# Kernel optimization log

Hardware: AMD Instinct MI355X
Metric: run time of the kernel (lower is better)

## Reference

```python
import jax, jax.numpy as jnp
import numpy as np

N, E, F_IN, C1, H1, C2, NUM_CLASSES, NUM_GRAPHS = 50000, 800000, 128, 64, 4, 128, 5, 32
NEG_SLOPE = 0.2


def gat_conv(x, W, att_src, att_dst, bias, src, dst, heads, out_ch):
    # x: [N, in], W: [in, heads*out_ch], att_*: [heads, out_ch], bias: [heads*out_ch]
    n = x.shape[0]
    h = (x @ W).reshape(n, heads, out_ch)                      # [N,H,C]
    a_src = jnp.sum(h * att_src, axis=-1)                      # [N,H]
    a_dst = jnp.sum(h * att_dst, axis=-1)                      # [N,H]
    alpha = a_src[src] + a_dst[dst]                            # [E,H]
    alpha = jax.nn.leaky_relu(alpha, NEG_SLOPE)
    # scatter-softmax over incoming edges of each dst node (every node has a self-loop)
    amax = jax.ops.segment_max(alpha, dst, num_segments=n)
    ealpha = jnp.exp(alpha - amax[dst])
    denom = jax.ops.segment_sum(ealpha, dst, num_segments=n)
    alpha = ealpha / (denom[dst] + 1e-16)                      # [E,H]
    msg = h[src] * alpha[..., None]                            # [E,H,C]
    out = jax.ops.segment_sum(msg, dst, num_segments=n)        # [N,H,C]
    return out.reshape(n, heads * out_ch) + bias


def setup_inputs() -> dict:
    key = jax.random.key(0)
    ks = jax.random.split(key, 12)
    x = jax.random.normal(ks[0], (N, F_IN), dtype=jnp.float32)
    edge_index = jax.random.randint(ks[1], (2, E), 0, N, dtype=jnp.int64)
    batch = jnp.sort(jax.random.randint(ks[2], (N,), 0, NUM_GRAPHS, dtype=jnp.int64))
    s1 = 1.0 / np.sqrt(F_IN)
    s2 = 1.0 / np.sqrt(H1 * C1)
    s3 = 1.0 / np.sqrt(C2)
    return {
        "x": x,
        "edge_index": edge_index,
        "batch": batch,
        "W1": jax.random.normal(ks[3], (F_IN, H1 * C1), dtype=jnp.float32) * s1,
        "att_src1": jax.random.normal(ks[4], (H1, C1), dtype=jnp.float32) * s1,
        "att_dst1": jax.random.normal(ks[5], (H1, C1), dtype=jnp.float32) * s1,
        "b1": jnp.zeros((H1 * C1,), dtype=jnp.float32),
        "W2": jax.random.normal(ks[6], (H1 * C1, C2), dtype=jnp.float32) * s2,
        "att_src2": jax.random.normal(ks[7], (1, C2), dtype=jnp.float32) * s2,
        "att_dst2": jax.random.normal(ks[8], (1, C2), dtype=jnp.float32) * s2,
        "b2": jnp.zeros((C2,), dtype=jnp.float32),
        "lin_w": jax.random.normal(ks[9], (C2, NUM_CLASSES), dtype=jnp.float32) * s3,
        "lin_b": jnp.zeros((NUM_CLASSES,), dtype=jnp.float32),
    }


def reference(x, edge_index, batch, W1, att_src1, att_dst1, b1, W2, att_src2, att_dst2, b2, lin_w, lin_b):
    n = x.shape[0]
    # PyG GATConv adds self-loops by default
    loops = jnp.arange(n, dtype=edge_index.dtype)
    src = jnp.concatenate([edge_index[0], loops])
    dst = jnp.concatenate([edge_index[1], loops])
    h = jax.nn.elu(gat_conv(x, W1, att_src1, att_dst1, b1, src, dst, H1, C1))
    h = jax.nn.elu(gat_conv(h, W2, att_src2, att_dst2, b2, src, dst, 1, C2))
    # global_mean_pool over graphs
    sums = jax.ops.segment_sum(h, batch, num_segments=NUM_GRAPHS)          # [G,C2]
    counts = jax.ops.segment_sum(jnp.ones((n,), h.dtype), batch, num_segments=NUM_GRAPHS)
    pooled = sums / jnp.maximum(counts, 1.0)[:, None]
    # dropout is identity in eval mode
    return pooled @ lin_w + lin_b
```

## Files before the change

### kernel.cpp

```cpp
#include <hip/hip_runtime.h>
#include <math.h>

#define NEG_SLOPE 0.2f

__device__ inline float lrelu(float x) { return x > 0.f ? x : NEG_SLOPE * x; }

typedef __attribute__((ext_vector_type(8))) _Float16 f16x8;
typedef __attribute__((ext_vector_type(4))) float f32x4;
typedef __attribute__((ext_vector_type(2))) float f32x2;
typedef __attribute__((ext_vector_type(4))) _Float16 h16x4;
typedef __attribute__((ext_vector_type(2))) _Float16 h16x2;

__global__ void convW_k(const float* __restrict__ W1, const float* __restrict__ W2,
                        _Float16* __restrict__ BT1, _Float16* __restrict__ BT2)
{
    int i = blockIdx.x * blockDim.x + threadIdx.x;
    if (i < 32768) {
        int n = i >> 7, k = i & 127;
        BT1[(size_t)n * 128 + k] = (_Float16)W1[(size_t)k * 256 + n];
    } else {
        int idx = i - 32768;
        int n = idx >> 8, k = idx & 255;
        BT2[(size_t)n * 256 + k] = (_Float16)W2[(size_t)k * 128 + n];
    }
}

template<int N, int K, int H, bool AF16>
__launch_bounds__(256)
__global__ void gemm_fused(const void* __restrict__ A, const _Float16* __restrict__ BT,
                           unsigned char* __restrict__ HB, const float* __restrict__ att_s,
                           const float* __restrict__ att_d, float* __restrict__ aS,
                           float* __restrict__ aD, int M)
{
    constexpr int ITERS = K / 32;
    constexpr int WN = N / 4;
    constexpr int NT = WN / 16;
    constexpr int NCH = (N * 4) / 256;
    __shared__ unsigned short As[64 * 40] __attribute__((aligned(16)));
    __shared__ unsigned short Bs[N * 40] __attribute__((aligned(16)));
    const int t = threadIdx.x;
    const int wave = t >> 6, lane = t & 63;
    const int quad = lane >> 4, l15 = lane & 15;
    const int rowBase = blockIdx.x * 64;

    f32x4 acc[4][NT];
#pragma unroll
    for (int mi = 0; mi < 4; ++mi)
#pragma unroll
        for (int ni = 0; ni < NT; ++ni)
            acc[mi][ni] = (f32x4){0.f, 0.f, 0.f, 0.f};

    const int ar = t >> 2;
    const int ak = (t & 3) << 3;
    const int bc = (t * NCH) >> 2;
    const int bks = (t * NCH) & 3;

    for (int it = 0; it < ITERS; ++it) {
        {
            int gr = rowBase + ar;
            f16x8 hv;
#pragma unroll
            for (int j = 0; j < 8; ++j) hv[j] = (_Float16)0.f;
            if (gr < M) {
                if constexpr (AF16) {
                    hv = *(const f16x8*)((const _Float16*)A + (size_t)gr * K + it * 32 + ak);
                } else {
                    const float* ap = (const float*)A + (size_t)gr * K + it * 32 + ak;
                    float4 v0 = *(const float4*)ap;
                    float4 v1 = *(const float4*)(ap + 4);
                    hv[0] = (_Float16)v0.x; hv[1] = (_Float16)v0.y;
                    hv[2] = (_Float16)v0.z; hv[3] = (_Float16)v0.w;
                    hv[4] = (_Float16)v1.x; hv[5] = (_Float16)v1.y;
                    hv[6] = (_Float16)v1.z; hv[7] = (_Float16)v1.w;
                }
            }
            *(f16x8*)&As[ar * 40 + ak] = hv;
        }
        {
            const _Float16* bp = BT + (size_t)bc * K + it * 32 + bks * 8;
            unsigned short* dp = &Bs[bc * 40 + bks * 8];
#pragma unroll
            for (int j = 0; j < NCH; ++j)
                *(f16x8*)(dp + j * 8) = *(const f16x8*)(bp + j * 8);
        }
        __syncthreads();
        f16x8 af[4], bfr[NT];
#pragma unroll
        for (int mi = 0; mi < 4; ++mi)
            af[mi] = *(const f16x8*)&As[(mi * 16 + l15) * 40 + quad * 8];
#pragma unroll
        for (int ni = 0; ni < NT; ++ni)
            bfr[ni] = *(const f16x8*)&Bs[(wave * WN + ni * 16 + l15) * 40 + quad * 8];
#pragma unroll
        for (int mi = 0; mi < 4; ++mi)
#pragma unroll
            for (int ni = 0; ni < NT; ++ni)
                acc[mi][ni] = __builtin_amdgcn_mfma_f32_16x16x32_f16(
                    af[mi], bfr[ni], acc[mi][ni], 0, 0, 0);
        __syncthreads();
    }
    float asv[NT], adv[NT];
#pragma unroll
    for (int ni = 0; ni < NT; ++ni) {
        int col = wave * WN + ni * 16 + l15;
        asv[ni] = att_s[col];
        adv[ni] = att_d[col];
    }
#pragma unroll
    for (int mi = 0; mi < 4; ++mi) {
#pragma unroll
        for (int r = 0; r < 4; ++r) {
            int row = rowBase + mi * 16 + quad * 4 + r;
            bool ok = row < M;
            float ss = 0.f, sd = 0.f;
#pragma unroll
            for (int ni = 0; ni < NT; ++ni) {
                float v = acc[mi][ni][r];
                ss += v * asv[ni];
                sd += v * adv[ni];
            }
#pragma unroll
            for (int ni = 0; ni < NT; ni += 2) {
                int pk = __builtin_amdgcn_cvt_pk_fp8_f32(acc[mi][ni][r],
                                                         acc[mi][ni + 1][r], 0, false);
                if (ok) {
                    HB[(size_t)row * N + wave * WN + ni * 16 + l15] =
                        (unsigned char)(pk & 0xff);
                    HB[(size_t)row * N + wave * WN + (ni + 1) * 16 + l15] =
                        (unsigned char)((pk >> 8) & 0xff);
                }
            }
#pragma unroll
            for (int off = 8; off > 0; off >>= 1) {
                ss += __shfl_xor(ss, off);
                sd += __shfl_xor(sd, off);
            }
            if (ok && l15 == 0) {
                if (H == 4) {
                    aS[row * 4 + wave] = ss;
                    aD[row * 4 + wave] = sd;
                } else {
                    atomicAdd(&aS[row], ss);
                    atomicAdd(&aD[row], sd);
                }
            }
        }
    }
}

#define BIN_EPT 32
__launch_bounds__(256)
__global__ void bcount_k(const int* __restrict__ dst, int* __restrict__ bcnt,
                         int ET, int E, int NBUCK)
{
    __shared__ int hist[1024];
    for (int i = threadIdx.x; i < NBUCK; i += 256) hist[i] = 0;
    __syncthreads();
    int e0 = blockIdx.x * (256 * BIN_EPT) + threadIdx.x;
#pragma unroll
    for (int j = 0; j < BIN_EPT; ++j) {
        int e = e0 + j * 256;
        if (e < ET) {
            int d = (e < E) ? dst[e] : (e - E);
            atomicAdd(&hist[d >> 6], 1);
        }
    }
    __syncthreads();
    for (int i = threadIdx.x; i < NBUCK; i += 256) {
        int c = hist[i];
        if (c > 0) atomicAdd(&bcnt[i], c);
    }
}

__global__ void bscan_k(const int* __restrict__ bcnt, int* __restrict__ bbase,
                        int* __restrict__ ccursor, int nb)
{
    __shared__ int sh[1024];
    int t = threadIdx.x;
    int v = (t < nb) ? bcnt[t] : 0;
    sh[t] = v;
    __syncthreads();
#pragma unroll
    for (int o = 1; o < 1024; o <<= 1) {
        int u = (t >= o) ? sh[t - o] : 0;
        __syncthreads();
        sh[t] += u;
        __syncthreads();
    }
    if (t < nb) {
        int excl = sh[t] - v;
        bbase[t] = excl;
        ccursor[t] = excl;
    }
    if (t == nb - 1) bbase[nb] = sh[t];
}

__launch_bounds__(256)
__global__ void binpass_k(const int* __restrict__ src, const int* __restrict__ dst,
                          int* __restrict__ ccursor, unsigned int* __restrict__ tmp,
                          int ET, int E, int NBUCK)
{
    __shared__ int hist[1024];
    for (int i = threadIdx.x; i < NBUCK; i += 256) hist[i] = 0;
    __syncthreads();
    int e0 = blockIdx.x * (256 * BIN_EPT) + threadIdx.x;
    unsigned int ev[BIN_EPT];
    int meta[BIN_EPT];
#pragma unroll
    for (int j = 0; j < BIN_EPT; ++j) {
        int e = e0 + j * 256;
        meta[j] = -1;
        if (e < ET) {
            int s, d;
            if (e < E) { s = src[e]; d = dst[e]; } else { s = e - E; d = s; }
            ev[j] = (unsigned int)s | ((unsigned int)d << 16);
            int b = d >> 6;
            int r = atomicAdd(&hist[b], 1);
            meta[j] = (r << 10) | b;
        }
    }
    __syncthreads();
    for (int i = threadIdx.x; i < NBUCK; i += 256) {
        int c = hist[i];
        hist[i] = (c > 0) ? atomicAdd(&ccursor[i], c) : 0;
    }
    __syncthreads();
#pragma unroll
    for (int j = 0; j < BIN_EPT; ++j) {
        if (meta[j] >= 0) {
            int b = meta[j] & 1023;
            int r = meta[j] >> 10;
            tmp[hist[b] + r] = ev[j];
        }
    }
}

__global__ void fine_k(const int* __restrict__ bbase, const unsigned int* __restrict__ tmp,
                       int* __restrict__ rowptr, unsigned short* __restrict__ esrc,
                       int Nn, int ET, int NBUCK)
{
    __shared__ int lcnt[64], lpre[64], lcur[64];
    int t = threadIdx.x;
    int b = blockIdx.x;
    int n0 = b << 6;
    int base = bbase[b];
    int end = bbase[b + 1];
    if (t < 64) lcnt[t] = 0;
    __syncthreads();
    for (int i = base + t; i < end; i += 256)
        atomicAdd(&lcnt[(tmp[i] >> 16) & 63], 1);
    __syncthreads();
    if (t < 64) lpre[t] = lcnt[t];
    __syncthreads();
#pragma unroll
    for (int o = 1; o < 64; o <<= 1) {
        int u = (t < 64 && t >= o) ? lpre[t - o] : 0;
        __syncthreads();
        if (t < 64) lpre[t] += u;
        __syncthreads();
    }
    if (t < 64) {
        int n = n0 + t;
        int excl = lpre[t] - lcnt[t];
        if (n < Nn) {
            rowptr[n] = base + excl;
            lcur[t] = base + excl;
        }
    }
    if (b == NBUCK - 1 && t == 0) rowptr[Nn] = ET;
    __syncthreads();
    for (int i = base + t; i < end; i += 256) {
        unsigned int v = tmp[i];
        int pos = atomicAdd(&lcur[(v >> 16) & 63], 1);
        esrc[pos] = (unsigned short)(v & 0xffffu);
    }
}

__global__ void gather1_k(const int* __restrict__ rp, const unsigned short* __restrict__ esrc,
                          const unsigned char* __restrict__ hb, const float* __restrict__ aS,
                          const float* __restrict__ aD, const float* __restrict__ bias,
                          _Float16* __restrict__ out, int Nn)
{
    int d = blockIdx.x * 4 + (threadIdx.x >> 6);
    int lane = threadIdx.x & 63;
    if (d >= Nn) return;
    int c4 = lane << 2;
    int head = lane >> 4;
    int p0 = __builtin_amdgcn_readfirstlane(rp[d]);
    int p1 = __builtin_amdgcn_readfirstlane(rp[d + 1]);
    float adh = aD[d * 4 + head];
    const float* aSh = aS + head;
    float m = -1e30f, den = 0.f;
    float ax = 0.f, ay = 0.f, az = 0.f, aw = 0.f;
    int p = p0;
    for (; p + 8 <= p1; p += 8) {
        int s[8];
#pragma unroll
        for (int j = 0; j < 8; ++j) s[j] = __builtin_amdgcn_readfirstlane(esrc[p + j]);
        unsigned int v[8];
#pragma unroll
        for (int j = 0; j < 8; ++j)
            v[j] = *(const unsigned int*)&hb[(size_t)s[j] * 256 + c4];
        float l[8];
#pragma unroll
        for (int j = 0; j < 8; ++j) l[j] = lrelu(aSh[s[j] * 4] + adh);
        float lm = l[0];
#pragma unroll
        for (int j = 1; j < 8; ++j) lm = fmaxf(lm, l[j]);
        if (lm > m) {
            float r = __expf(m - lm);
            ax *= r; ay *= r; az *= r; aw *= r; den *= r;
            m = lm;
        }
#pragma unroll
        for (int j = 0; j < 8; ++j) {
            float w = __expf(l[j] - m);
            den += w;
            f32x2 lo = __builtin_amdgcn_cvt_pk_f32_fp8((int)v[j], false);
            f32x2 hi = __builtin_amdgcn_cvt_pk_f32_fp8((int)v[j], true);
            ax += lo[0] * w;
            ay += lo[1] * w;
            az += hi[0] * w;
            aw += hi[1] * w;
        }
    }
    int rem = p1 - p;
    if (rem > 0) {
        int s[8];
        unsigned int v[8];
        float l[8];
#pragma unroll
        for (int j = 0; j < 8; ++j)
            if (j < rem) s[j] = __builtin_amdgcn_readfirstlane(esrc[p + j]);
#pragma unroll
        for (int j = 0; j < 8; ++j)
            if (j < rem) v[j] = *(const unsigned int*)&hb[(size_t)s[j] * 256 + c4];
#pragma unroll
        for (int j = 0; j < 8; ++j) l[j] = -1e30f;
#pragma unroll
        for (int j = 0; j < 8; ++j)
            if (j < rem) l[j] = lrelu(aSh[s[j] * 4] + adh);
        float lm = l[0];
#pragma unroll
        for (int j = 1; j < 8; ++j) lm = fmaxf(lm, l[j]);
        if (lm > m) {
            float r = __expf(m - lm);
            ax *= r; ay *= r; az *= r; aw *= r; den *= r;
            m = lm;
        }
#pragma unroll
        for (int j = 0; j < 8; ++j) {
            if (j < rem) {
                float w = __expf(l[j] - m);
                den += w;
                f32x2 lo = __builtin_amdgcn_cvt_pk_f32_fp8((int)v[j], false);
                f32x2 hi = __builtin_amdgcn_cvt_pk_f32_fp8((int)v[j], true);
                ax += lo[0] * w;
                ay += lo[1] * w;
                az += hi[0] * w;
                aw += hi[1] * w;
            }
        }
    }
    float inv = 1.f / (den + 1e-16f);
    float4 b4 = *(const float4*)&bias[c4];
    float rx, ry, rz, rw;
    rx = ax * inv + b4.x; rx = rx > 0.f ? rx : expm1f(rx);
    ry = ay * inv + b4.y; ry = ry > 0.f ? ry : expm1f(ry);
    rz = az * inv + b4.z; rz = rz > 0.f ? rz : expm1f(rz);
    rw = aw * inv + b4.w; rw = rw > 0.f ? rw : expm1f(rw);
    h16x4 r16;
    r16[0] = (_Float16)rx; r16[1] = (_Float16)ry;
    r16[2] = (_Float16)rz; r16[3] = (_Float16)rw;
    *(h16x4*)&out[(size_t)d * 256 + c4] = r16;
}

__global__ void gather2_k(const int* __restrict__ rp, const unsigned short* __restrict__ esrc,
                          const unsigned char* __restrict__ hb, const float* __restrict__ aS,
                          const float* __restrict__ aD, _Float16* __restrict__ out, int Nn)
{
    int d = blockIdx.x * 4 + (threadIdx.x >> 6);
    int lane = threadIdx.x & 63;
    if (d >= Nn) return;
    int c2 = lane << 1;
    int p0 = __builtin_amdgcn_readfirstlane(rp[d]);
    int p1 = __builtin_amdgcn_readfirstlane(rp[d + 1]);
    float adh = aD[d];
    float m = -1e30f, den = 0.f;
    float ax = 0.f, ay = 0.f;
    int p = p0;
    for (; p + 8 <= p1; p += 8) {
        int s[8];
#pragma unroll
        for (int j = 0; j < 8; ++j) s[j] = __builtin_amdgcn_readfirstlane(esrc[p + j]);
        unsigned short v[8];
#pragma unroll
        for (int j = 0; j < 8; ++j)
            v[j] = *(const unsigned short*)&hb[(size_t)s[j] * 128 + c2];
        float l[8];
#pragma unroll
        for (int j = 0; j < 8; ++j) l[j] = lrelu(aS[s[j]] + adh);
        float lm = l[0];
#pragma unroll
        for (int j = 1; j < 8; ++j) lm = fmaxf(lm, l[j]);
        if (lm > m) {
            float r = __expf(m - lm);
            ax *= r; ay *= r; den *= r;
            m = lm;
        }
#pragma unroll
        for (int j = 0; j < 8; ++j) {
            float w = __expf(l[j] - m);
            den += w;
            f32x2 lo = __builtin_amdgcn_cvt_pk_f32_fp8((int)v[j], false);
            ax += lo[0] * w;
            ay += lo[1] * w;
        }
    }
    int rem = p1 - p;
    if (rem > 0) {
        int s[8];
        unsigned short v[8];
        float l[8];
#pragma unroll
        for (int j = 0; j < 8; ++j)
            if (j < rem) s[j] = __builtin_amdgcn_readfirstlane(esrc[p + j]);
#pragma unroll
        for (int j = 0; j < 8; ++j)
            if (j < rem) v[j] = *(const unsigned short*)&hb[(size_t)s[j] * 128 + c2];
#pragma unroll
        for (int j = 0; j < 8; ++j) l[j] = -1e30f;
#pragma unroll
        for (int j = 0; j < 8; ++j)
            if (j < rem) l[j] = lrelu(aS[s[j]] + adh);
        float lm = l[0];
#pragma unroll
        for (int j = 1; j < 8; ++j) lm = fmaxf(lm, l[j]);
        if (lm > m) {
            float r = __expf(m - lm);
            ax *= r; ay *= r; den *= r;
            m = lm;
        }
#pragma unroll
        for (int j = 0; j < 8; ++j) {
            if (j < rem) {
                float w = __expf(l[j] - m);
                den += w;
                f32x2 lo = __builtin_amdgcn_cvt_pk_f32_fp8((int)v[j], false);
                ax += lo[0] * w;
                ay += lo[1] * w;
            }
        }
    }
    float inv = 1.f / (den + 1e-16f);
    h16x2 r16;
    r16[0] = (_Float16)(ax * inv);
    r16[1] = (_Float16)(ay * inv);
    *(h16x2*)&out[(size_t)d * 128 + c2] = r16;
}

__global__ void pool_k(const _Float16* __restrict__ o2, const float* __restrict__ b2,
                       const int* __restrict__ batch, float* __restrict__ sums, int Nn, int C)
{
    int c = threadIdx.x;
    int n0 = blockIdx.x * 64;
    int n1 = min(n0 + 64, Nn);
    float local = 0.f;
    int gcur = batch[n0];
    float bc = b2[c];
    for (int n = n0; n < n1; ++n) {
        int g = batch[n];
        if (g != gcur) {
            atomicAdd(&sums[gcur * C + c], local);
            local = 0.f;
            gcur = g;
        }
        float v = (float)o2[(size_t)n * C + c] + bc;
        local += v > 0.f ? v : expm1f(v);
    }
    atomicAdd(&sums[gcur * C + c], local);
}

__global__ void final_k(const float* __restrict__ sums, const int* __restrict__ batch,
                        const float* __restrict__ lin_w, const float* __restrict__ lin_b,
                        float* __restrict__ out, int Nn, int G, int C, int NC)
{
    __shared__ float inv[64];
    int t = threadIdx.x;
    if (t < G) {
        int lo = 0, hi = Nn;
        while (lo < hi) { int mid = (lo + hi) >> 1; if (batch[mid] < t) lo = mid + 1; else hi = mid; }
        int lb = lo;
        lo = 0; hi = Nn;
        while (lo < hi) { int mid = (lo + hi) >> 1; if (batch[mid] < t + 1) lo = mid + 1; else hi = mid; }
        int cnt = lo - lb;
        inv[t] = 1.f / fmaxf((float)cnt, 1.f);
    }
    __syncthreads();
    if (t < G * NC) {
        int g = t / NC, k = t % NC;
        float acc = 0.f;
        for (int c = 0; c < C; ++c) acc += sums[g * C + c] * lin_w[c * NC + k];
        out[t] = acc * inv[g] + lin_b[k];
    }
}

extern "C" void kernel_launch(void* const* d_in, const int* in_sizes, int n_in,
                              void* d_out, int out_size, void* d_ws, size_t ws_size,
                              hipStream_t stream)
{
    const float* x      = (const float*)d_in[0];
    const int*   eidx   = (const int*)d_in[1];
    const int*   batch  = (const int*)d_in[2];
    const float* W1     = (const float*)d_in[3];
    const float* att_s1 = (const float*)d_in[4];
    const float* att_d1 = (const float*)d_in[5];
    const float* b1     = (const float*)d_in[6];
    const float* W2     = (const float*)d_in[7];
    const float* att_s2 = (const float*)d_in[8];
    const float* att_d2 = (const float*)d_in[9];
    const float* b2     = (const float*)d_in[10];
    const float* lin_w  = (const float*)d_in[11];
    const float* lin_b  = (const float*)d_in[12];

    const int Nn  = in_sizes[2];
    const int E   = in_sizes[1] / 2;
    const int H1_ = 4, C1_ = 64, C2_ = 128, G = 32, NC = 5;
    const int D1 = H1_ * C1_;
    const int ET = E + Nn;
    const int NBUCK = (Nn + 63) >> 6;

    const int* srcp = eidx;
    const int* dstp = eidx + E;

    float* ws = (float*)d_ws;
    size_t off = 0;
    auto alloc = [&](size_t n) { float* p = ws + off; off += n; return p; };
    _Float16* o1h = (_Float16*)alloc((size_t)Nn * D1 / 2);
    _Float16* o2h = (_Float16*)alloc((size_t)Nn * C2_ / 2);
    float* aS1  = alloc((size_t)Nn * H1_);
    float* aD1  = alloc((size_t)Nn * H1_);
    float* aS2  = alloc(Nn);
    float* aD2  = alloc(Nn);
    float* sums = alloc((size_t)G * C2_);
    _Float16* BT1 = (_Float16*)alloc(D1 * 128 / 2);
    _Float16* BT2 = (_Float16*)alloc(C2_ * 256 / 2);
    unsigned char* hb1 = (unsigned char*)alloc((size_t)Nn * D1 / 4);
    unsigned char* hb2 = (unsigned char*)alloc((size_t)Nn * C2_ / 4);
    int* iws    = (int*)(ws + off);
    int* rowptr = iws;
    int* bcnt   = iws + Nn + 1;
    int* bbase  = iws + Nn + 1 + 1024;
    int* ccursor= iws + Nn + 1 + 2049;
    unsigned int* tmp = (unsigned int*)(iws + Nn + 1 + 2049 + 1024);
    unsigned short* esrc = (unsigned short*)(tmp + ET);

    const int GB = (Nn + 63) / 64;
    const int BINB = (ET + 256 * BIN_EPT - 1) / (256 * BIN_EPT);

    hipMemsetAsync(bcnt, 0, 1024 * 4, stream);
    hipMemsetAsync(aS2, 0, (size_t)2 * Nn * 4, stream);
    bcount_k<<<BINB, 256, 0, stream>>>(dstp, bcnt, ET, E, NBUCK);
    bscan_k<<<1, 1024, 0, stream>>>(bcnt, bbase, ccursor, NBUCK);
    binpass_k<<<BINB, 256, 0, stream>>>(srcp, dstp, ccursor, tmp, ET, E, NBUCK);
    fine_k<<<NBUCK, 256, 0, stream>>>(bbase, tmp, rowptr, esrc, Nn, ET, NBUCK);

    convW_k<<<256, 256, 0, stream>>>(W1, W2, BT1, BT2);

    gemm_fused<256, 128, 4, false><<<GB, 256, 0, stream>>>(x, BT1, hb1, att_s1, att_d1,
                                                           aS1, aD1, Nn);
    gather1_k<<<(Nn + 3) / 4, 256, 0, stream>>>(rowptr, esrc, hb1, aS1, aD1, b1, o1h, Nn);

    gemm_fused<128, 256, 1, true><<<GB, 256, 0, stream>>>(o1h, BT2, hb2, att_s2, att_d2,
                                                          aS2, aD2, Nn);
    gather2_k<<<(Nn + 3) / 4, 256, 0, stream>>>(rowptr, esrc, hb2, aS2, aD2, o2h, Nn);

    hipMemsetAsync(sums, 0, (size_t)G * C2_ * 4, stream);
    pool_k<<<GB, C2_, 0, stream>>>(o2h, b2, batch, sums, Nn, C2_);
    final_k<<<1, 256, 0, stream>>>(sums, batch, lin_w, lin_b, (float*)d_out, Nn, G, C2_, NC);
}
```

Baseline: 319.2 us.

## Precompute per-edge softmax weights in a separate alpha kernel before gathers

Adds an alpha_k kernel that computes each destination's max attention logit with a wave reduction and writes exp(logit - max) per edge as fp16, stored separately per head. The gather kernels then read these precomputed weights instead of recomputing leaky-relu, the online max and the rescaling exp inside their inner loops. This strips the serial online-softmax bookkeeping and redundant per-lane exp work from the gathers. In exchange it adds two extra kernel launches plus an extra write and read of the per-edge weight arrays, and stores the weights in reduced fp16 precision.

```diff
diff --git a/kernel.cpp b/kernel.cpp
--- a/kernel.cpp
+++ b/kernel.cpp
@@ -276,21 +276,66 @@
     }
 }
 
+template<int H>
+__global__ void alpha_k(const int* __restrict__ rp, const unsigned short* __restrict__ esrc,
+                        const float* __restrict__ aS, const float* __restrict__ aD,
+                        _Float16* __restrict__ wout, int ET, int Nn)
+{
+    int d = blockIdx.x * 4 + (threadIdx.x >> 6);
+    int lane = threadIdx.x & 63;
+    if (d >= Nn) return;
+    int p0 = __builtin_amdgcn_readfirstlane(rp[d]);
+    int p1 = __builtin_amdgcn_readfirstlane(rp[d + 1]);
+    float adh[H];
+#pragma unroll
+    for (int h = 0; h < H; ++h) adh[h] = aD[d * H + h];
+    float m[H];
+#pragma unroll
+    for (int h = 0; h < H; ++h) m[h] = -1e30f;
+    for (int p = p0 + lane; p < p1; p += 64) {
+        int s = esrc[p];
+        if (H == 4) {
+            float4 a4 = *(const float4*)&aS[s * 4];
+            m[0] = fmaxf(m[0], lrelu(a4.x + adh[0]));
+            m[1] = fmaxf(m[1], lrelu(a4.y + adh[1]));
+            m[2] = fmaxf(m[2], lrelu(a4.z + adh[2]));
+            m[3] = fmaxf(m[3], lrelu(a4.w + adh[3]));
+        } else {
+            m[0] = fmaxf(m[0], lrelu(aS[s] + adh[0]));
+        }
+    }
+#pragma unroll
+    for (int h = 0; h < H; ++h)
+#pragma unroll
+        for (int off = 32; off > 0; off >>= 1)
+            m[h] = fmaxf(m[h], __shfl_xor(m[h], off));
+    for (int p = p0 + lane; p < p1; p += 64) {
+        int s = esrc[p];
+        if (H == 4) {
+            float4 a4 = *(const float4*)&aS[s * 4];
+            wout[p] = (_Float16)__expf(lrelu(a4.x + adh[0]) - m[0]);
+            wout[(size_t)ET + p] = (_Float16)__expf(lrelu(a4.y + adh[1]) - m[1]);
+            wout[(size_t)2 * ET + p] = (_Float16)__expf(lrelu(a4.z + adh[2]) - m[2]);
+            wout[(size_t)3 * ET + p] = (_Float16)__expf(lrelu(a4.w + adh[3]) - m[3]);
+        } else {
+            wout[p] = (_Float16)__expf(lrelu(aS[s] + adh[0]) - m[0]);
+        }
+    }
+}
+
 __global__ void gather1_k(const int* __restrict__ rp, const unsigned short* __restrict__ esrc,
-                          const unsigned char* __restrict__ hb, const float* __restrict__ aS,
-                          const float* __restrict__ aD, const float* __restrict__ bias,
-                          _Float16* __restrict__ out, int Nn)
+                          const unsigned char* __restrict__ hb, const _Float16* __restrict__ wv,
+                          const float* __restrict__ bias, _Float16* __restrict__ out,
+                          int ET, int Nn)
 {
     int d = blockIdx.x * 4 + (threadIdx.x >> 6);
     int lane = threadIdx.x & 63;
     if (d >= Nn) return;
     int c4 = lane << 2;
-    int head = lane >> 4;
+    const _Float16* wh = wv + (size_t)(lane >> 4) * ET;
     int p0 = __builtin_amdgcn_readfirstlane(rp[d]);
     int p1 = __builtin_amdgcn_readfirstlane(rp[d + 1]);
-    float adh = aD[d * 4 + head];
-    const float* aSh = aS + head;
-    float m = -1e30f, den = 0.f;
+    float den = 0.f;
     float ax = 0.f, ay = 0.f, az = 0.f, aw = 0.f;
     int p = p0;
     for (; p + 8 <= p1; p += 8) {
@@ -301,34 +346,25 @@
 #pragma unroll
         for (int j = 0; j < 8; ++j)
             v[j] = *(const unsigned int*)&hb[(size_t)s[j] * 256 + c4];
-        float l[8];
-#pragma unroll
-        for (int j = 0; j < 8; ++j) l[j] = lrelu(aSh[s[j] * 4] + adh);
-        float lm = l[0];
-#pragma unroll
-        for (int j = 1; j < 8; ++j) lm = fmaxf(lm, l[j]);
-        if (lm > m) {
-            float r = __expf(m - lm);
-            ax *= r; ay *= r; az *= r; aw *= r; den *= r;
-            m = lm;
-        }
+        float w[8];
+#pragma unroll
+        for (int j = 0; j < 8; ++j) w[j] = (float)wh[p + j];
 #pragma unroll
         for (int j = 0; j < 8; ++j) {
-            float w = __expf(l[j] - m);
-            den += w;
+            den += w[j];
             f32x2 lo = __builtin_amdgcn_cvt_pk_f32_fp8((int)v[j], false);
             f32x2 hi = __builtin_amdgcn_cvt_pk_f32_fp8((int)v[j], true);
-            ax += lo[0] * w;
-            ay += lo[1] * w;
-            az += hi[0] * w;
-            aw += hi[1] * w;
+            ax += lo[0] * w[j];
+            ay += lo[1] * w[j];
+            az += hi[0] * w[j];
+            aw += hi[1] * w[j];
         }
     }
     int rem = p1 - p;
     if (rem > 0) {
         int s[8];
         unsigned int v[8];
-        float l[8];
+        float w[8];
 #pragma unroll
         for (int j = 0; j < 8; ++j)
             if (j < rem) s[j] = __builtin_amdgcn_readfirstlane(esrc[p + j]);
@@ -336,29 +372,18 @@
         for (int j = 0; j < 8; ++j)
             if (j < rem) v[j] = *(const unsigned int*)&hb[(size_t)s[j] * 256 + c4];
 #pragma unroll
-        for (int j = 0; j < 8; ++j) l[j] = -1e30f;
-#pragma unroll
-        for (int j = 0; j < 8; ++j)
-            if (j < rem) l[j] = lrelu(aSh[s[j] * 4] + adh);
-        float lm = l[0];
-#pragma unroll
-        for (int j = 1; j < 8; ++j) lm = fmaxf(lm, l[j]);
-        if (lm > m) {
-            float r = __expf(m - lm);
-            ax *= r; ay *= r; az *= r; aw *= r; den *= r;
-            m = lm;
-        }
+        for (int j = 0; j < 8; ++j)
+            if (j < rem) w[j] = (float)wh[p + j];
 #pragma unroll
         for (int j = 0; j < 8; ++j) {
             if (j < rem) {
-                float w = __expf(l[j] - m);
-                den += w;
+                den += w[j];
                 f32x2 lo = __builtin_amdgcn_cvt_pk_f32_fp8((int)v[j], false);
                 f32x2 hi = __builtin_amdgcn_cvt_pk_f32_fp8((int)v[j], true);
-                ax += lo[0] * w;
-                ay += lo[1] * w;
-                az += hi[0] * w;
-                aw += hi[1] * w;
+                ax += lo[0] * w[j];
+                ay += lo[1] * w[j];
+                az += hi[0] * w[j];
+                aw += hi[1] * w[j];
             }
         }
     }
@@ -376,8 +401,8 @@
 }
 
 __global__ void gather2_k(const int* __restrict__ rp, const unsigned short* __restrict__ esrc,
-                          const unsigned char* __restrict__ hb, const float* __restrict__ aS,
-                          const float* __restrict__ aD, _Float16* __restrict__ out, int Nn)
+                          const unsigned char* __restrict__ hb, const _Float16* __restrict__ wv,
+                          _Float16* __restrict__ out, int ET, int Nn)
 {
     int d = blockIdx.x * 4 + (threadIdx.x >> 6);
     int lane = threadIdx.x & 63;
@@ -385,8 +410,7 @@
     int c2 = lane << 1;
     int p0 = __builtin_amdgcn_readfirstlane(rp[d]);
     int p1 = __builtin_amdgcn_readfirstlane(rp[d + 1]);
-    float adh = aD[d];
-    float m = -1e30f, den = 0.f;
+    float den = 0.f;
     float ax = 0.f, ay = 0.f;
     int p = p0;
     for (; p + 8 <= p1; p += 8) {
@@ -397,31 +421,22 @@
 #pragma unroll
         for (int j = 0; j < 8; ++j)
             v[j] = *(const unsigned short*)&hb[(size_t)s[j] * 128 + c2];
-        float l[8];
-#pragma unroll
-        for (int j = 0; j < 8; ++j) l[j] = lrelu(aS[s[j]] + adh);
-        float lm = l[0];
-#pragma unroll
-        for (int j = 1; j < 8; ++j) lm = fmaxf(lm, l[j]);
-        if (lm > m) {
-            float r = __expf(m - lm);
-            ax *= r; ay *= r; den *= r;
-            m = lm;
-        }
+        float w[8];
+#pragma unroll
+        for (int j = 0; j < 8; ++j) w[j] = (float)wv[p + j];
 #pragma unroll
         for (int j = 0; j < 8; ++j) {
-            float w = __expf(l[j] - m);
-            den += w;
+            den += w[j];
             f32x2 lo = __builtin_amdgcn_cvt_pk_f32_fp8((int)v[j], false);
-            ax += lo[0] * w;
-            ay += lo[1] * w;
+            ax += lo[0] * w[j];
+            ay += lo[1] * w[j];
         }
     }
     int rem = p1 - p;
     if (rem > 0) {
         int s[8];
         unsigned short v[8];
-        float l[8];
+        float w[8];
 #pragma unroll
         for (int j = 0; j < 8; ++j)
             if (j < rem) s[j] = __builtin_amdgcn_readfirstlane(esrc[p + j]);
@@ -429,26 +444,15 @@
         for (int j = 0; j < 8; ++j)
             if (j < rem) v[j] = *(const unsigned short*)&hb[(size_t)s[j] * 128 + c2];
 #pragma unroll
-        for (int j = 0; j < 8; ++j) l[j] = -1e30f;
-#pragma unroll
-        for (int j = 0; j < 8; ++j)
-            if (j < rem) l[j] = lrelu(aS[s[j]] + adh);
-        float lm = l[0];
-#pragma unroll
-        for (int j = 1; j < 8; ++j) lm = fmaxf(lm, l[j]);
-        if (lm > m) {
-            float r = __expf(m - lm);
-            ax *= r; ay *= r; den *= r;
-            m = lm;
-        }
+        for (int j = 0; j < 8; ++j)
+            if (j < rem) w[j] = (float)wv[p + j];
 #pragma unroll
         for (int j = 0; j < 8; ++j) {
             if (j < rem) {
-                float w = __expf(l[j] - m);
-                den += w;
+                den += w[j];
                 f32x2 lo = __builtin_amdgcn_cvt_pk_f32_fp8((int)v[j], false);
-                ax += lo[0] * w;
-                ay += lo[1] * w;
+                ax += lo[0] * w[j];
+                ay += lo[1] * w[j];
             }
         }
     }
@@ -547,6 +551,8 @@
     _Float16* BT2 = (_Float16*)alloc(C2_ * 256 / 2);
     unsigned char* hb1 = (unsigned char*)alloc((size_t)Nn * D1 / 4);
     unsigned char* hb2 = (unsigned char*)alloc((size_t)Nn * C2_ / 4);
+    _Float16* w1h = (_Float16*)alloc((size_t)2 * ET + 16);
+    _Float16* w2h = (_Float16*)alloc((size_t)ET / 2 + 16);
     int* iws    = (int*)(ws + off);
     int* rowptr = iws;
     int* bcnt   = iws + Nn + 1;
@@ -556,6 +562,7 @@
     unsigned short* esrc = (unsigned short*)(tmp + ET);
 
     const int GB = (Nn + 63) / 64;
+    const int NW = (Nn + 3) / 4;
     const int BINB = (ET + 256 * BIN_EPT - 1) / (256 * BIN_EPT);
 
     hipMemsetAsync(bcnt, 0, 1024 * 4, stream);
@@ -569,11 +576,13 @@
 
     gemm_fused<256, 128, 4, false><<<GB, 256, 0, stream>>>(x, BT1, hb1, att_s1, att_d1,
                                                            aS1, aD1, Nn);
-    gather1_k<<<(Nn + 3) / 4, 256, 0, stream>>>(rowptr, esrc, hb1, aS1, aD1, b1, o1h, Nn);
+    alpha_k<4><<<NW, 256, 0, stream>>>(rowptr, esrc, aS1, aD1, w1h, ET, Nn);
+    gather1_k<<<NW, 256, 0, stream>>>(rowptr, esrc, hb1, w1h, b1, o1h, ET, Nn);
 
     gemm_fused<128, 256, 1, true><<<GB, 256, 0, stream>>>(o1h, BT2, hb2, att_s2, att_d2,
                                                           aS2, aD2, Nn);
-    gather2_k<<<(Nn + 3) / 4, 256, 0, stream>>>(rowptr, esrc, hb2, aS2, aD2, o2h, Nn);
+    alpha_k<1><<<NW, 256, 0, stream>>>(rowptr, esrc, aS2, aD2, w2h, ET, Nn);
+    gather2_k<<<NW, 256, 0, stream>>>(rowptr, esrc, hb2, w2h, o2h, ET, Nn);
 
     hipMemsetAsync(sums, 0, (size_t)G * C2_ * 4, stream);
     pool_k<<<GB, C2_, 0, stream>>>(o2h, b2, batch, sums, Nn, C2_);
```

Result: slower. 354.0 us (+10.9%).
